# Kernel optimization log

Hardware: AMD Instinct MI355X
Metric: run time of the kernel (lower is better)

## Reference

```python
import jax, jax.numpy as jnp
import numpy as np

N = 4096
D = 256
DEG = 32
E0 = N * DEG
RATIO = 0.5
NEG_SLOPE = 0.2


def setup_inputs() -> dict:
    key = jax.random.key(0)
    ks = jax.random.split(key, 12)
    # edges with NO self loops (so appending all N self-loops == add_remaining_self_loops)
    src = jax.random.randint(ks[0], (E0,), 0, N, dtype=jnp.int32)
    off = jax.random.randint(ks[1], (E0,), 1, N, dtype=jnp.int32)
    dst = ((src + off) % N).astype(jnp.int32)
    edge_index = jnp.stack([src, dst])
    edge_weight = jnp.ones((E0,), jnp.float32)
    x = jax.random.normal(ks[2], (N, D), jnp.float32)
    s = 1.0 / np.sqrt(D)
    u = lambda k, shp: jax.random.uniform(k, shp, jnp.float32, -s, s)
    return {
        'x': x,
        'edge_index': edge_index,
        'edge_weight': edge_weight,
        'lin_w': u(ks[3], (D, D)), 'lin_b': u(ks[4], (D,)),
        'att_w': jax.random.uniform(ks[5], (2 * D, 1), jnp.float32, -1.0 / np.sqrt(2 * D), 1.0 / np.sqrt(2 * D)),
        'att_b': u(ks[6], (1,)),
        'le1_w': u(ks[7], (D, 1)), 'le1_b': u(ks[8], (1,)),
        'le2_w': u(ks[9], (D, 1)),
        'le3_w': u(ks[10], (D, 1)), 'le3_b': u(ks[11], (1,)),
    }


def reference(x, edge_index, edge_weight, lin_w, lin_b, att_w, att_b,
              le1_w, le1_b, le2_w, le3_w, le3_b):
    n, d = x.shape
    # add_remaining_self_loops (input has no self loops by construction)
    loop = jnp.arange(n, dtype=edge_index.dtype)
    src = jnp.concatenate([edge_index[0], loop])
    dst = jnp.concatenate([edge_index[1], loop])
    w = jnp.concatenate([edge_weight, jnp.ones((n,), edge_weight.dtype)])

    # GNN is None -> x_pool = x
    x_pool_j = x[src]                                        # [E, D] gather
    x_q = jax.ops.segment_max(x_pool_j, dst, num_segments=n)  # scatter-max
    x_q_e = (x_q @ lin_w + lin_b)[dst]                        # [E, D]
    # att(cat([x_q, x_pool_j])) without materializing [E, 2D]
    score = x_q_e @ att_w[:d, 0] + x_pool_j @ att_w[d:, 0] + att_b[0]
    score = jax.nn.leaky_relu(score, NEG_SLOPE)
    # segment softmax over destination nodes
    smax = jax.ops.segment_max(score, dst, num_segments=n)
    ex = jnp.exp(score - smax[dst])
    denom = jax.ops.segment_sum(ex, dst, num_segments=n)
    score = ex / denom[dst]
    # dropout p=0 -> no-op
    xn = jax.ops.segment_sum(x_pool_j * score[:, None], dst, num_segments=n)

    # LEConv fitness: sigmoid( lin3(x) + sum_j (lin1(x_j) - lin2(x_i)) )
    a = xn @ le1_w + le1_b          # [N, 1]
    b = xn @ le2_w                  # [N, 1] (no bias)
    agg = jax.ops.segment_sum(a[src] - b[dst], dst, num_segments=n)
    fitness = jax.nn.sigmoid((agg + xn @ le3_w + le3_b)[:, 0])

    k = int(np.ceil(RATIO * N))
    _, perm = jax.lax.top_k(fitness, k)
    x_out = xn[perm] * fitness[perm][:, None]

    # Coarsening A_c = S[:, perm]^T @ A @ S[:, perm]; dense since SpGEMM nnz is data-dependent
    S = jnp.zeros((n, n), x.dtype).at[src, dst].add(score)[:, perm]  # [N, k]
    A = jnp.zeros((n, n), x.dtype).at[src, dst].add(w)               # [N, N]
    A_c = S.T @ (A @ S)                                              # [k, k]
    A_c = A_c * (1.0 - jnp.eye(k, dtype=A_c.dtype))                  # remove_diag
    return x_out, A_c, perm
```

## Files before the change

kernel.cpp:

```cpp
#include <hip/hip_runtime.h>
#include <cstdint>
#include <cstddef>
#include <math.h>

#define NN   4096
#define DD   256
#define E0S  131072
#define NE   (E0S + NN)
#define KK   2048
#define NEG_SLOPE 0.2f
#define SEGCAP 256

typedef float floatx4 __attribute__((ext_vector_type(4)));

__device__ __forceinline__ int esrc(const int* s, int e){ return e < E0S ? s[e] : e - E0S; }
__device__ __forceinline__ int edst(const int* d, int e){ return e < E0S ? d[e] : e - E0S; }

__global__ void init_kernel(int* deg_dst, int* deg_src, int* colmap, float* Ac, int zero_ac){
    int i = blockIdx.x * blockDim.x + threadIdx.x;
    int stride = gridDim.x * blockDim.x;
    if (zero_ac){
        for (size_t t = i; t < (size_t)KK * KK; t += stride) Ac[t] = 0.f;
    }
    for (int t = i; t < NN; t += stride){ deg_dst[t] = 0; deg_src[t] = 0; colmap[t] = -1; }
}

__global__ void count_kernel(const int* e_src, const int* e_dst, int* deg_dst, int* deg_src){
    int e = blockIdx.x * blockDim.x + threadIdx.x;
    if (e < NE){
        atomicAdd(&deg_dst[edst(e_dst, e)], 1);
        atomicAdd(&deg_src[esrc(e_src, e)], 1);
    }
}

__global__ void __launch_bounds__(1024) scan_kernel(const int* degA, int* offA, int* curA,
                                                    const int* degB, int* offB, int* curB){
    const int* deg = (blockIdx.x == 0) ? degA : degB;
    int* off = (blockIdx.x == 0) ? offA : offB;
    int* cur = (blockIdx.x == 0) ? curA : curB;
    __shared__ int part[1024];
    int t = threadIdx.x;
    int base = t * 4;
    int s0 = deg[base], s1 = deg[base+1], s2 = deg[base+2], s3 = deg[base+3];
    int tot = s0 + s1 + s2 + s3;
    part[t] = tot;
    __syncthreads();
    for (int d = 1; d < 1024; d <<= 1){
        int v = (t >= d) ? part[t - d] : 0;
        __syncthreads();
        part[t] += v;
        __syncthreads();
    }
    int excl = part[t] - tot;
    off[base]   = excl;            cur[base]   = excl;
    off[base+1] = excl + s0;       cur[base+1] = excl + s0;
    off[base+2] = excl + s0 + s1;  cur[base+2] = excl + s0 + s1;
    off[base+3] = excl + s0 + s1 + s2; cur[base+3] = excl + s0 + s1 + s2;
    if (t == 1023) off[NN] = part[1023];
}

__global__ void fill_kernel(const int* e_src, const int* e_dst, int* cur_dst, int* cur_src,
                            int* eid_dst, int* eid_src){
    int e = blockIdx.x * blockDim.x + threadIdx.x;
    if (e < NE){
        int p = atomicAdd(&cur_dst[edst(e_dst, e)], 1); eid_dst[p] = e;
        int q = atomicAdd(&cur_src[esrc(e_src, e)], 1); eid_src[q] = e;
    }
}

__global__ void segsort_kernel(const int* off_dst, int* eid_dst, const int* off_src, int* eid_src,
                               const int* e_src, int* isd){
    __shared__ int buf[4][SEGCAP];
    int wid  = (blockIdx.x * blockDim.x + threadIdx.x) >> 6;
    int lane = threadIdx.x & 63;
    int w    = threadIdx.x >> 6;
    const int* off; int* eid; int n; bool isdst;
    if (wid < NN){ off = off_dst; eid = eid_dst; n = wid; isdst = true; }
    else         { off = off_src; eid = eid_src; n = wid - NN; isdst = false; }
    int lo = off[n], hi = off[n+1];
    int L = hi - lo;
    int Lc = (L <= SEGCAP) ? L : SEGCAP;
    for (int i = lane; i < Lc; i += 64) buf[w][i] = eid[lo + i];
    __syncthreads();
    if (L <= SEGCAP){
        for (int i = lane; i < L; i += 64){
            int v = buf[w][i];
            int r = 0;
            for (int j = 0; j < L; ++j) r += (buf[w][j] < v);
            eid[lo + r] = v;
            if (isdst) isd[lo + r] = esrc(e_src, v);
        }
    } else if (lane == 0){
        for (int i = lo + 1; i < hi; ++i){
            int v = eid[i]; int j = i - 1;
            while (j >= lo && eid[j] > v){ eid[j+1] = eid[j]; --j; }
            eid[j+1] = v;
        }
        if (isdst) for (int i = lo; i < hi; ++i) isd[i] = esrc(e_src, eid[i]);
    }
}

#define LROWS 8
__global__ void sml_kernel(const float* x, const int* off, const int* isd,
                           const float* lin_w, const float* lin_b, const float* att_w,
                           float* q_s, float* p_s){
    __shared__ float xs[LROWS][DD];
    __shared__ int   is_[SEGCAP];
    __shared__ float s1[256], s2[256];
    int col = threadIdx.x;
    int r0 = blockIdx.x * LROWS;
    for (int r = 0; r < LROWS; ++r){
        int n = r0 + r;
        int lo = off[n], hi = off[n+1];
        int L = hi - lo;
        int Ls = (L <= SEGCAP) ? L : SEGCAP;
        for (int t = col; t < Ls; t += 256) is_[t] = isd[lo + t];
        __syncthreads();
        float m = -INFINITY;
        int t = 0;
        for (; t + 1 < Ls; t += 2){
            float v0 = x[(size_t)is_[t]   * DD + col];
            float v1 = x[(size_t)is_[t+1] * DD + col];
            m = fmaxf(m, fmaxf(v0, v1));
        }
        if (t < Ls) m = fmaxf(m, x[(size_t)is_[t] * DD + col]);
        for (t = Ls; t < L; ++t)
            m = fmaxf(m, x[(size_t)isd[lo + t] * DD + col]);
        xs[r][col] = m;
        __syncthreads();
    }
    float acc[LROWS];
    float bc = lin_b[col];
    #pragma unroll
    for (int r = 0; r < LROWS; ++r) acc[r] = bc;
    for (int kk = 0; kk < DD; ++kk){
        float wv = lin_w[(size_t)kk * DD + col];
        #pragma unroll
        for (int r = 0; r < LROWS; ++r) acc[r] = fmaf(xs[r][kk], wv, acc[r]);
    }
    float aw1 = att_w[col];
    float aw2 = att_w[DD + col];
    for (int r = 0; r < LROWS; ++r){
        int n = r0 + r;
        s1[col] = acc[r] * aw1;
        s2[col] = x[(size_t)n * DD + col] * aw2;
        __syncthreads();
        for (int d = 128; d > 0; d >>= 1){
            if (col < d){ s1[col] += s1[col + d]; s2[col] += s2[col + d]; }
            __syncthreads();
        }
        if (col == 0){ q_s[n] = s1[0]; p_s[n] = s2[0]; }
        __syncthreads();
    }
}

__global__ void softxn_kernel(const float* x, const int* off, const int* eid, const int* isd,
                              const float* q_s, const float* p_s, const float* att_b,
                              const float* le1_w, const float* le1_b, const float* le2_w,
                              const float* le3_w, const float* le3_b,
                              float* sc, float* ssd, float* xn,
                              float* a_, float* b_, float* c_){
    __shared__ int   is_[SEGCAP];
    __shared__ float ss_[SEGCAP];
    __shared__ float s1[256], s2[256], s3[256];
    int n = blockIdx.x, col = threadIdx.x;
    int lo = off[n], hi = off[n+1];
    int L = hi - lo;
    int Ls = (L <= SEGCAP) ? L : SEGCAP;
    for (int t = col; t < Ls; t += 256) is_[t] = isd[lo + t];
    __syncthreads();
    if (col < 64){
        int lane = col;
        float ab = att_b[0];
        float qn = q_s[n];
        float m = -INFINITY;
        for (int t = lane; t < L; t += 64){
            int sn = (t < Ls) ? is_[t] : isd[lo + t];
            float s = qn + p_s[sn] + ab;
            s = (s > 0.f) ? s : NEG_SLOPE * s;
            m = fmaxf(m, s);
        }
        #pragma unroll
        for (int d = 32; d > 0; d >>= 1) m = fmaxf(m, __shfl_xor(m, d));
        float sum = 0.f;
        for (int t = lane; t < L; t += 64){
            int sn = (t < Ls) ? is_[t] : isd[lo + t];
            float s = qn + p_s[sn] + ab;
            s = (s > 0.f) ? s : NEG_SLOPE * s;
            float ex = expf(s - m);
            if (t < Ls) ss_[t] = ex; else ssd[lo + t] = ex;
            sum += ex;
        }
        #pragma unroll
        for (int d = 32; d > 0; d >>= 1) sum += __shfl_xor(sum, d);
        float inv = 1.f / sum;
        for (int t = lane; t < L; t += 64){
            float v = ((t < Ls) ? ss_[t] : ssd[lo + t]) * inv;
            if (t < Ls) ss_[t] = v;
            ssd[lo + t] = v;
            sc[eid[lo + t]] = v;
        }
    }
    __syncthreads();
    float acc = 0.f;
    int t = 0;
    for (; t + 1 < Ls; t += 2){
        float v0 = x[(size_t)is_[t]   * DD + col];
        float v1 = x[(size_t)is_[t+1] * DD + col];
        acc = fmaf(ss_[t],   v0, acc);
        acc = fmaf(ss_[t+1], v1, acc);
    }
    if (t < Ls) acc = fmaf(ss_[t], x[(size_t)is_[t] * DD + col], acc);
    for (t = Ls; t < L; ++t)
        acc = fmaf(ssd[lo + t], x[(size_t)isd[lo + t] * DD + col], acc);
    xn[(size_t)n * DD + col] = acc;
    s1[col] = acc * le1_w[col];
    s2[col] = acc * le2_w[col];
    s3[col] = acc * le3_w[col];
    __syncthreads();
    for (int dd = 128; dd > 0; dd >>= 1){
        if (col < dd){ s1[col] += s1[col+dd]; s2[col] += s2[col+dd]; s3[col] += s3[col+dd]; }
        __syncthreads();
    }
    if (col == 0){
        a_[n] = s1[0] + le1_b[0];
        b_[n] = s2[0];
        c_[n] = s3[0] + le3_b[0];
    }
}

__global__ void fitness_kernel(const int* off, const int* isd,
                               const float* a_, const float* b_, const float* c_,
                               float* fit){
    int wave = threadIdx.x >> 6;
    int lane = threadIdx.x & 63;
    int n = blockIdx.x * 4 + wave;
    int lo = off[n], hi = off[n+1];
    float bn = b_[n];
    float s = 0.f;
    for (int t = lo + lane; t < hi; t += 64){
        s += a_[isd[t]] - bn;
    }
    #pragma unroll
    for (int d = 32; d > 0; d >>= 1) s += __shfl_xor(s, d);
    if (lane == 0){
        float z = s + c_[n];
        fit[n] = 1.f / (1.f + expf(-z));
    }
}

__global__ void __launch_bounds__(1024) topk_kernel(const float* fit, int* perm, int* colmap,
                                                    float* out_perm){
    __shared__ unsigned long long keys[NN];
    int t = threadIdx.x;
    for (int i = t; i < NN; i += 1024){
        unsigned int u = __float_as_uint(fit[i]);
        u = (u & 0x80000000u) ? ~u : (u | 0x80000000u);
        u = ~u;
        keys[i] = ((unsigned long long)u << 32) | (unsigned int)i;
    }
    __syncthreads();
    for (unsigned int ssize = 2; ssize <= NN; ssize <<= 1){
        for (unsigned int stride = ssize >> 1; stride > 0; stride >>= 1){
            for (int i = t; i < NN / 2; i += 1024){
                unsigned int idx = 2u * i - (i & (stride - 1u));
                unsigned int par = idx + stride;
                bool asc = ((idx & ssize) == 0u);
                unsigned long long a = keys[idx], b = keys[par];
                if ((a > b) == asc){ keys[idx] = b; keys[par] = a; }
            }
            __syncthreads();
        }
    }
    for (int i = t; i < KK; i += 1024){
        int node = (int)(keys[i] & 0xFFFFFFFFull);
        perm[i] = node;
        colmap[node] = i;
        out_perm[i] = (float)node;
    }
}

__global__ void xoutprep_kernel(const float* xn, const float* fit, const int* perm, float* x_out,
                                const int* eid_src, const int* e_dst, const int* colmap,
                                const float* sc, int* cp, float* sp){
    int b = blockIdx.x;
    if (b < KK){
        int r = b, d = threadIdx.x;
        int p = perm[r];
        x_out[(size_t)r * DD + d] = xn[(size_t)p * DD + d] * fit[p];
    } else {
        int u = (b - KK) * 256 + threadIdx.x;
        if (u < NE){
            int f = eid_src[u];
            cp[u] = colmap[edst(e_dst, f)];
            sp[u] = sc[f];
        }
    }
}

__global__ void spgemm1_kernel(const int* e_dst, const float* ew,
                               const int* off_src, const int* eid_src,
                               const int* cp, const float* sp, float* T){
    __shared__ float row[KK];
    __shared__ int   jlo_[SEGCAP];
    __shared__ int   jhi_[SEGCAP];
    __shared__ float w_[SEGCAP];
    int i = blockIdx.x;
    for (int c = threadIdx.x; c < KK; c += 256) row[c] = 0.f;
    int lo = off_src[i], hi = off_src[i+1];
    int L = hi - lo;
    int Ls = (L <= SEGCAP) ? L : SEGCAP;
    for (int t = threadIdx.x; t < Ls; t += 256){
        int e = eid_src[lo + t];
        int j = edst(e_dst, e);
        jlo_[t] = off_src[j];
        jhi_[t] = off_src[j+1];
        w_[t]   = (e < E0S) ? ew[e] : 1.0f;
    }
    __syncthreads();
    int sw = threadIdx.x >> 5, ln = threadIdx.x & 31;
    for (int t = sw; t < Ls; t += 8){
        float w1 = w_[t];
        for (int u = jlo_[t] + ln; u < jhi_[t]; u += 32){
            int c = cp[u];
            if (c >= 0) atomicAdd(&row[c], w1 * sp[u]);
        }
    }
    for (int t = Ls + sw; t < L; t += 8){
        int e = eid_src[lo + t];
        int j = edst(e_dst, e);
        float w1 = (e < E0S) ? ew[e] : 1.0f;
        int jlo = off_src[j], jhi = off_src[j+1];
        for (int u = jlo + ln; u < jhi; u += 32){
            int c = cp[u];
            if (c >= 0) atomicAdd(&row[c], w1 * sp[u]);
        }
    }
    __syncthreads();
    float* Trow = T + (size_t)i * KK;
    for (int c = threadIdx.x; c < KK; c += 256) Trow[c] = row[c];
}

__global__ void spgemm2_kernel(const int* perm, const int* off_dst,
                               const int* isd, const float* ssd,
                               const float* T, float* Ac){
    __shared__ int   is_[8][SEGCAP];
    __shared__ float ss_[8][SEGCAP];
    int bx = blockIdx.x;
    int by = blockIdx.y;
    int half = by >> 8;
    int rr   = by & 255;
    int sub  = threadIdx.x >> 5;
    int lane = threadIdx.x & 31;
    int r = rr * 8 + sub;
    int chunk = bx + 8 * half;
    int c0 = chunk * 128 + lane * 4;
    int node = perm[r];
    int lo = off_dst[node], hi = off_dst[node+1];
    int L = hi - lo;
    int Ls = (L <= SEGCAP) ? L : SEGCAP;
    for (int t = lane; t < Ls; t += 32){
        is_[sub][t] = isd[lo + t];
        ss_[sub][t] = ssd[lo + t];
    }
    __syncthreads();
    floatx4 acc = {0.f, 0.f, 0.f, 0.f};
    int t = 0;
    for (; t + 1 < Ls; t += 2){
        floatx4 a = *(const floatx4*)&T[(size_t)is_[sub][t]   * KK + c0];
        floatx4 b = *(const floatx4*)&T[(size_t)is_[sub][t+1] * KK + c0];
        float s0 = ss_[sub][t], s1 = ss_[sub][t+1];
        acc.x = fmaf(s0, a.x, acc.x); acc.y = fmaf(s0, a.y, acc.y);
        acc.z = fmaf(s0, a.z, acc.z); acc.w = fmaf(s0, a.w, acc.w);
        acc.x = fmaf(s1, b.x, acc.x); acc.y = fmaf(s1, b.y, acc.y);
        acc.z = fmaf(s1, b.z, acc.z); acc.w = fmaf(s1, b.w, acc.w);
    }
    for (; t < Ls; ++t){
        floatx4 a = *(const floatx4*)&T[(size_t)is_[sub][t] * KK + c0];
        float s0 = ss_[sub][t];
        acc.x = fmaf(s0, a.x, acc.x); acc.y = fmaf(s0, a.y, acc.y);
        acc.z = fmaf(s0, a.z, acc.z); acc.w = fmaf(s0, a.w, acc.w);
    }
    for (t = Ls; t < L; ++t){
        floatx4 a = *(const floatx4*)&T[(size_t)isd[lo + t] * KK + c0];
        float s0 = ssd[lo + t];
        acc.x = fmaf(s0, a.x, acc.x); acc.y = fmaf(s0, a.y, acc.y);
        acc.z = fmaf(s0, a.z, acc.z); acc.w = fmaf(s0, a.w, acc.w);
    }
    if (r - c0 >= 0 && r - c0 < 4){
        if (r - c0 == 0) acc.x = 0.f;
        else if (r - c0 == 1) acc.y = 0.f;
        else if (r - c0 == 2) acc.z = 0.f;
        else acc.w = 0.f;
    }
    __builtin_nontemporal_store(acc, (floatx4*)&Ac[(size_t)r * KK + c0]);
}

__global__ void ac_kernel(const int* e_src, const int* e_dst, const float* ew,
                          const int* off_src,
                          const int* cp, const float* sp, float* Ac){
    int e1 = blockIdx.x * blockDim.x + threadIdx.x;
    if (e1 >= NE) return;
    int i = (e1 < E0S) ? e_src[e1] : e1 - E0S;
    int j = (e1 < E0S) ? e_dst[e1] : e1 - E0S;
    float w1 = (e1 < E0S) ? ew[e1] : 1.0f;
    int ilo = off_src[i], ihi = off_src[i+1];
    int jlo = off_src[j], jhi = off_src[j+1];
    for (int ta = ilo; ta < ihi; ++ta){
        int ca = cp[ta];
        if (ca < 0) continue;
        float va = sp[ta] * w1;
        float* rowp = Ac + (size_t)ca * KK;
        for (int tb = jlo; tb < jhi; ++tb){
            int cb = cp[tb];
            if (cb < 0) continue;
            atomicAdd(&rowp[cb], va * sp[tb]);
        }
    }
}

__global__ void diag_kernel(float* Ac){
    int r = blockIdx.x * blockDim.x + threadIdx.x;
    if (r < KK) Ac[(size_t)r * KK + r] = 0.f;
}

extern "C" void kernel_launch(void* const* d_in, const int* in_sizes, int n_in,
                              void* d_out, int out_size, void* d_ws, size_t ws_size,
                              hipStream_t stream){
    const float* x     = (const float*)d_in[0];
    const int*   ei    = (const int*)d_in[1];
    const float* ew    = (const float*)d_in[2];
    const float* lin_w = (const float*)d_in[3];
    const float* lin_b = (const float*)d_in[4];
    const float* att_w = (const float*)d_in[5];
    const float* att_b = (const float*)d_in[6];
    const float* le1_w = (const float*)d_in[7];
    const float* le1_b = (const float*)d_in[8];
    const float* le2_w = (const float*)d_in[9];
    const float* le3_w = (const float*)d_in[10];
    const float* le3_b = (const float*)d_in[11];

    const int* e_src = ei;
    const int* e_dst = ei + E0S;

    float* out    = (float*)d_out;
    float* x_out  = out;
    float* Ac     = out + (size_t)KK * DD;
    float* operm  = out + (size_t)KK * DD + (size_t)KK * KK;

    char* wp = (char*)d_ws;
    auto alloc_i = [&](size_t n){ int* p = (int*)wp; wp += n * sizeof(int); return p; };
    auto alloc_f = [&](size_t n){ float* p = (float*)wp; wp += n * sizeof(float); return p; };

    int* deg_dst = alloc_i(NN);
    int* deg_src = alloc_i(NN);
    int* off_dst = alloc_i(NN + 1);
    int* off_src = alloc_i(NN + 1);
    int* cur_dst = alloc_i(NN);
    int* cur_src = alloc_i(NN);
    int* eid_dst = alloc_i(NE);
    int* eid_src = alloc_i(NE);
    int* colmap  = alloc_i(NN);
    int* perm    = alloc_i(KK);
    int* isd     = alloc_i(NE);
    int* cp      = alloc_i(NE);
    float* sp    = alloc_f(NE);
    float* ssd   = alloc_f(NE);
    float* q_s   = alloc_f(NN);
    float* p_s   = alloc_f(NN);
    float* a_    = alloc_f(NN);
    float* b_    = alloc_f(NN);
    float* c_    = alloc_f(NN);
    float* fit   = alloc_f(NN);
    float* sc    = alloc_f(NE);
    float* xn    = alloc_f((size_t)NN * DD);
    float* T     = alloc_f((size_t)NN * KK);
    bool dense_ok = ((size_t)(wp - (char*)d_ws) <= ws_size);
    (void)n_in; (void)in_sizes; (void)out_size;

    const int EB = (NE + 255) / 256;

    init_kernel<<<2048, 256, 0, stream>>>(deg_dst, deg_src, colmap, Ac, dense_ok ? 0 : 1);
    count_kernel<<<EB, 256, 0, stream>>>(e_src, e_dst, deg_dst, deg_src);
    scan_kernel<<<2, 1024, 0, stream>>>(deg_dst, off_dst, cur_dst, deg_src, off_src, cur_src);
    fill_kernel<<<EB, 256, 0, stream>>>(e_src, e_dst, cur_dst, cur_src, eid_dst, eid_src);
    segsort_kernel<<<(2 * NN) / 4, 256, 0, stream>>>(off_dst, eid_dst, off_src, eid_src, e_src, isd);
    sml_kernel<<<NN / LROWS, 256, 0, stream>>>(x, off_dst, isd, lin_w, lin_b, att_w, q_s, p_s);
    softxn_kernel<<<NN, 256, 0, stream>>>(x, off_dst, eid_dst, isd, q_s, p_s, att_b,
                                          le1_w, le1_b, le2_w, le3_w, le3_b,
                                          sc, ssd, xn, a_, b_, c_);
    fitness_kernel<<<NN / 4, 256, 0, stream>>>(off_dst, isd, a_, b_, c_, fit);
    topk_kernel<<<1, 1024, 0, stream>>>(fit, perm, colmap, operm);
    xoutprep_kernel<<<KK + EB, 256, 0, stream>>>(xn, fit, perm, x_out,
                                                 eid_src, e_dst, colmap, sc, cp, sp);
    if (dense_ok){
        spgemm1_kernel<<<NN, 256, 0, stream>>>(e_dst, ew, off_src, eid_src, cp, sp, T);
        spgemm2_kernel<<<dim3(8, 512), 256, 0, stream>>>(perm, off_dst, isd, ssd, T, Ac);
    } else {
        ac_kernel<<<EB, 256, 0, stream>>>(e_src, e_dst, ew, off_src, cp, sp, Ac);
        diag_kernel<<<(KK + 255) / 256, 256, 0, stream>>>(Ac);
    }
}
```

Baseline: 231.6 us.

## Split segment-max gather from linear projection into separate kernels

The fused segment-max plus linear kernel is split in two. The first kernel has one wavefront per destination node and uses float4 vectorized gathers to write x_q to a new global buffer. The second kernel does the linear layer and attention dot products on 4 rows per block instead of 8, which gives more blocks. This aims to expose more parallelism for the latency-bound gather, at the cost of an extra launch, a 4 MB intermediate round trip, and less reuse of lin_w per block.

```diff
diff --git a/kernel.cpp b/kernel.cpp
--- a/kernel.cpp
+++ b/kernel.cpp
@@ -100,47 +100,62 @@
     }
 }
 
-#define LROWS 8
-__global__ void sml_kernel(const float* x, const int* off, const int* isd,
-                           const float* lin_w, const float* lin_b, const float* att_w,
-                           float* q_s, float* p_s){
-    __shared__ float xs[LROWS][DD];
-    __shared__ int   is_[SEGCAP];
+__global__ void segmax_kernel(const float* x, const int* off, const int* isd, float* x_q){
+    __shared__ int is_[4][SEGCAP];
+    int g = threadIdx.x >> 6;
+    int l = threadIdx.x & 63;
+    int n = blockIdx.x * 4 + g;
+    int lo = off[n], hi = off[n+1];
+    int L = hi - lo;
+    int Ls = (L <= SEGCAP) ? L : SEGCAP;
+    for (int t = l; t < Ls; t += 64) is_[g][t] = isd[lo + t];
+    __syncthreads();
+    int c0 = l * 4;
+    floatx4 m = {-INFINITY, -INFINITY, -INFINITY, -INFINITY};
+    int t = 0;
+    for (; t + 1 < Ls; t += 2){
+        floatx4 v0 = *(const floatx4*)&x[(size_t)is_[g][t]   * DD + c0];
+        floatx4 v1 = *(const floatx4*)&x[(size_t)is_[g][t+1] * DD + c0];
+        m.x = fmaxf(m.x, fmaxf(v0.x, v1.x));
+        m.y = fmaxf(m.y, fmaxf(v0.y, v1.y));
+        m.z = fmaxf(m.z, fmaxf(v0.z, v1.z));
+        m.w = fmaxf(m.w, fmaxf(v0.w, v1.w));
+    }
+    if (t < Ls){
+        floatx4 v0 = *(const floatx4*)&x[(size_t)is_[g][t] * DD + c0];
+        m.x = fmaxf(m.x, v0.x); m.y = fmaxf(m.y, v0.y);
+        m.z = fmaxf(m.z, v0.z); m.w = fmaxf(m.w, v0.w);
+    }
+    for (t = Ls; t < L; ++t){
+        floatx4 v0 = *(const floatx4*)&x[(size_t)isd[lo + t] * DD + c0];
+        m.x = fmaxf(m.x, v0.x); m.y = fmaxf(m.y, v0.y);
+        m.z = fmaxf(m.z, v0.z); m.w = fmaxf(m.w, v0.w);
+    }
+    *(floatx4*)&x_q[(size_t)n * DD + c0] = m;
+}
+
+#define LR2 4
+__global__ void linnd_kernel(const float* x, const float* x_q,
+                             const float* lin_w, const float* lin_b, const float* att_w,
+                             float* q_s, float* p_s){
+    __shared__ float xs[LR2][DD];
     __shared__ float s1[256], s2[256];
     int col = threadIdx.x;
-    int r0 = blockIdx.x * LROWS;
-    for (int r = 0; r < LROWS; ++r){
-        int n = r0 + r;
-        int lo = off[n], hi = off[n+1];
-        int L = hi - lo;
-        int Ls = (L <= SEGCAP) ? L : SEGCAP;
-        for (int t = col; t < Ls; t += 256) is_[t] = isd[lo + t];
-        __syncthreads();
-        float m = -INFINITY;
-        int t = 0;
-        for (; t + 1 < Ls; t += 2){
-            float v0 = x[(size_t)is_[t]   * DD + col];
-            float v1 = x[(size_t)is_[t+1] * DD + col];
-            m = fmaxf(m, fmaxf(v0, v1));
-        }
-        if (t < Ls) m = fmaxf(m, x[(size_t)is_[t] * DD + col]);
-        for (t = Ls; t < L; ++t)
-            m = fmaxf(m, x[(size_t)isd[lo + t] * DD + col]);
-        xs[r][col] = m;
-        __syncthreads();
-    }
-    float acc[LROWS];
+    int r0 = blockIdx.x * LR2;
+    for (int r = 0; r < LR2; ++r) xs[r][col] = x_q[(size_t)(r0 + r) * DD + col];
+    __syncthreads();
+    float acc[LR2];
     float bc = lin_b[col];
     #pragma unroll
-    for (int r = 0; r < LROWS; ++r) acc[r] = bc;
+    for (int r = 0; r < LR2; ++r) acc[r] = bc;
     for (int kk = 0; kk < DD; ++kk){
         float wv = lin_w[(size_t)kk * DD + col];
         #pragma unroll
-        for (int r = 0; r < LROWS; ++r) acc[r] = fmaf(xs[r][kk], wv, acc[r]);
+        for (int r = 0; r < LR2; ++r) acc[r] = fmaf(xs[r][kk], wv, acc[r]);
     }
     float aw1 = att_w[col];
     float aw2 = att_w[DD + col];
-    for (int r = 0; r < LROWS; ++r){
+    for (int r = 0; r < LR2; ++r){
         int n = r0 + r;
         s1[col] = acc[r] * aw1;
         s2[col] = x[(size_t)n * DD + col] * aw2;
@@ -473,6 +488,7 @@
     float* c_    = alloc_f(NN);
     float* fit   = alloc_f(NN);
     float* sc    = alloc_f(NE);
+    float* x_q   = alloc_f((size_t)NN * DD);
     float* xn    = alloc_f((size_t)NN * DD);
     float* T     = alloc_f((size_t)NN * KK);
     bool dense_ok = ((size_t)(wp - (char*)d_ws) <= ws_size);
@@ -485,7 +501,8 @@
     scan_kernel<<<2, 1024, 0, stream>>>(deg_dst, off_dst, cur_dst, deg_src, off_src, cur_src);
     fill_kernel<<<EB, 256, 0, stream>>>(e_src, e_dst, cur_dst, cur_src, eid_dst, eid_src);
     segsort_kernel<<<(2 * NN) / 4, 256, 0, stream>>>(off_dst, eid_dst, off_src, eid_src, e_src, isd);
-    sml_kernel<<<NN / LROWS, 256, 0, stream>>>(x, off_dst, isd, lin_w, lin_b, att_w, q_s, p_s);
+    segmax_kernel<<<NN / 4, 256, 0, stream>>>(x, off_dst, isd, x_q);
+    linnd_kernel<<<NN / LR2, 256, 0, stream>>>(x, x_q, lin_w, lin_b, att_w, q_s, p_s);
     softxn_kernel<<<NN, 256, 0, stream>>>(x, off_dst, eid_dst, isd, q_s, p_s, att_b,
                                           le1_w, le1_b, le2_w, le3_w, le3_b,
                                           sc, ssd, xn, a_, b_, c_);
```

Result: faster. 212.7 us (-8.2%).
